# Kernel tuning notes

Measured on AMD Instinct MI355X. Metric: run time of the kernel, lower is better.

Reference implementation:

```python
import jax, jax.numpy as jnp
import numpy as np

B, N, K_NEIGHBORS = 8, 2048, 16

def setup_inputs() -> dict:
    key = jax.random.key(0)
    k1, k2, k3 = jax.random.split(key, 3)
    distance_matrix = jax.random.uniform(k1, (B, N, N), dtype=jnp.float32)
    time_window_compatibility = jax.random.randint(k2, (B, N, N), 0, 2).astype(jnp.int32)
    depot = jax.random.randint(k3, (B, N), 0, 2).astype(jnp.int32)
    # graph.max_dist: per-batch max pairwise distance, broadcastable over [B,N,N]
    max_dist = jnp.max(distance_matrix.reshape(B, -1), axis=1).reshape(B, 1, 1)
    return {
        "distance_matrix": distance_matrix,
        "max_dist": max_dist,
        "time_window_compatibility": time_window_compatibility,
        "depot": depot,
        "num_neighbors_encoder": K_NEIGHBORS,
    }


def reference(distance_matrix, max_dist, time_window_compatibility, depot, num_neighbors_encoder):
    """Faithful JAX port of Actor.compute_encoder_mask.

    distance_matrix:            [B, N, N] float
    max_dist:                   [B, 1, 1] float
    time_window_compatibility:  [B, N, N] int 0/1
    depot:                      [B, N]    int 0/1
    num_neighbors_encoder:      python int (K)
    returns mask:               [B, N, N] float 0/1
    """
    dtype = distance_matrix.dtype
    b, n, _ = distance_matrix.shape

    twnc = (1 - time_window_compatibility).astype(dtype)          # time-window NON-compatibility
    diag = jnp.eye(n, dtype=dtype)                                  # [N,N], broadcasts over batch
    m = ((twnc + diag) > 0).astype(dtype)                           # blocked pairs for KNN

    # Push blocked pairs far away, then take K smallest distances per row.
    dist = distance_matrix * (1.0 - m) + m * max_dist * 10.0
    k = min(n, int(num_neighbors_encoder))
    neighbors_index = jax.lax.top_k(-dist, k)[1]                    # [B, N, K] smallest-dist indices

    # neighbors_mask[b,i,j] = 1 iff j is among the K nearest neighbors of i.
    bi = jnp.arange(b)[:, None, None]
    ii = jnp.arange(n)[None, :, None]
    neighbors_mask = jnp.zeros((b, n, n), dtype).at[bi, ii, neighbors_index].add(1.0)

    m2 = (twnc == 0).astype(dtype)                                  # time-window compatible pairs
    neighbs_time_mask = neighbors_mask * m2

    depot_f = depot.astype(dtype)
    depot_mask = ((depot_f[:, None, :] + depot_f[:, :, None]) > 0).astype(dtype)

    mask = ((neighbs_time_mask + depot_mask + diag) > 0).astype(dtype)
    return mask
```

## Files before the change

### kernel.cpp

```cpp
#include <hip/hip_runtime.h>
#include <stdint.h>

#define NN 2048
#define TPB 256
#define EPT 8
#define KNB 16
#define CAP 128
#define CAPPAD (CAP + 8)

static constexpr unsigned long long EXCL = ~0ull;
static constexpr unsigned long long T0KEY = ((unsigned long long)0x3D400000u) << 11;

__global__ __launch_bounds__(TPB) void encoder_mask_kernel(
    const float* __restrict__ D,
    const int*   __restrict__ TWC,
    const int*   __restrict__ depot,
    float*       __restrict__ out)
{
    const int row = blockIdx.x;
    const int b   = row >> 11;
    const int i   = row & (NN - 1);
    const int t   = threadIdx.x;
    const int j0  = t * EPT;

    float*       orow   = out + (size_t)row * NN;
    const int*   deprow = depot + b * NN;

    const int4 p0 = reinterpret_cast<const int4*>(deprow + j0)[0];
    const int4 p1 = reinterpret_cast<const int4*>(deprow + j0)[1];
    const int  depot_i = deprow[i];

    if (depot_i != 0) {
        const float4 ones = make_float4(1.f, 1.f, 1.f, 1.f);
        float4* o4 = reinterpret_cast<float4*>(orow + j0);
        o4[0] = ones;
        o4[1] = ones;
        return;
    }

    const float* drow = D   + (size_t)row * NN;
    const int*   trow = TWC + (size_t)row * NN;

    const float4 d0 = reinterpret_cast<const float4*>(drow + j0)[0];
    const float4 d1 = reinterpret_cast<const float4*>(drow + j0)[1];
    const int4   c0 = reinterpret_cast<const int4*>(trow + j0)[0];
    const int4   c1 = reinterpret_cast<const int4*>(trow + j0)[1];

    __shared__ unsigned long long cand[CAPPAD];
    __shared__ unsigned long long selq[TPB];
    __shared__ unsigned long long wpart[2][TPB / 64];
    __shared__ int cnt;

    selq[t] = 0ull;
    if (t < CAPPAD) cand[t] = EXCL;
    if (t == 0) cnt = 0;
    __syncthreads();

    const float dv[EPT] = {d0.x, d0.y, d0.z, d0.w, d1.x, d1.y, d1.z, d1.w};
    const int   cv[EPT] = {c0.x, c0.y, c0.z, c0.w, c1.x, c1.y, c1.z, c1.w};

    unsigned long long key[EPT];
    #pragma unroll
    for (int k = 0; k < EPT; ++k) {
        const int j = j0 + k;
        const bool excl = (cv[k] == 0) | (j == i);
        key[k] = excl ? EXCL
                      : ((((unsigned long long)__float_as_uint(dv[k])) << 11) |
                         (unsigned long long)(unsigned)j);
    }

    int nloc = 0;
    #pragma unroll
    for (int k = 0; k < EPT; ++k) nloc += (key[k] < T0KEY) ? 1 : 0;

    if (nloc > 0) {
        int idx = atomicAdd(&cnt, nloc);
        #pragma unroll
        for (int k = 0; k < EPT; ++k) {
            if (key[k] < T0KEY) {
                if (idx < CAP) cand[idx] = key[k];
                ++idx;
            }
        }
    }
    __syncthreads();

    const int c = cnt;

    if (c >= KNB && c <= CAP) {
        if (t < c) {
            const unsigned long long mykey = cand[t];
            int rank = 0;
            const int cround = (c + 7) & ~7;
            #pragma unroll 1
            for (int q = 0; q < cround; q += 8) {
                const ulonglong2 a0 = *reinterpret_cast<const ulonglong2*>(&cand[q]);
                const ulonglong2 a1 = *reinterpret_cast<const ulonglong2*>(&cand[q + 2]);
                const ulonglong2 a2 = *reinterpret_cast<const ulonglong2*>(&cand[q + 4]);
                const ulonglong2 a3 = *reinterpret_cast<const ulonglong2*>(&cand[q + 6]);
                rank += (a0.x < mykey) ? 1 : 0;
                rank += (a0.y < mykey) ? 1 : 0;
                rank += (a1.x < mykey) ? 1 : 0;
                rank += (a1.y < mykey) ? 1 : 0;
                rank += (a2.x < mykey) ? 1 : 0;
                rank += (a2.y < mykey) ? 1 : 0;
                rank += (a3.x < mykey) ? 1 : 0;
                rank += (a3.y < mykey) ? 1 : 0;
            }
            if (rank < KNB) {
                reinterpret_cast<unsigned char*>(selq)[(int)(mykey & 2047u)] = 1;
            }
        }
    } else {
        const int wave = t >> 6;
        const int lane = t & 63;
        unsigned long long lmin = key[0];
        #pragma unroll
        for (int k = 1; k < EPT; ++k) lmin = (key[k] < lmin) ? key[k] : lmin;

        #pragma unroll 1
        for (int it = 0; it < KNB; ++it) {
            unsigned long long w = lmin;
            #pragma unroll
            for (int off = 32; off >= 1; off >>= 1) {
                const unsigned long long o = __shfl_xor(w, off);
                w = (o < w) ? o : w;
            }
            const int p = it & 1;
            if (lane == 0) wpart[p][wave] = w;
            __syncthreads();
            unsigned long long g = wpart[p][0];
            {
                const unsigned long long g1 = wpart[p][1];
                const unsigned long long g2 = wpart[p][2];
                const unsigned long long g3 = wpart[p][3];
                g = (g1 < g) ? g1 : g;
                g = (g2 < g) ? g2 : g;
                g = (g3 < g) ? g3 : g;
            }
            if (g == EXCL) break;
            const int jwin = (int)(g & 2047u);
            if (t == 0) reinterpret_cast<unsigned char*>(selq)[jwin] = 1;
            if (lmin == g) {
                unsigned long long nm = EXCL;
                #pragma unroll
                for (int k = 0; k < EPT; ++k) {
                    if (key[k] == g) key[k] = EXCL;
                    nm = (key[k] < nm) ? key[k] : nm;
                }
                lmin = nm;
            }
        }
    }
    __syncthreads();

    const unsigned long long selbits = selq[t];
    const int dpv[EPT] = {p0.x, p0.y, p0.z, p0.w, p1.x, p1.y, p1.z, p1.w};

    float ov[EPT];
    #pragma unroll
    for (int k = 0; k < EPT; ++k) {
        const int j = j0 + k;
        const bool sel = ((selbits >> (8 * k)) & 0xffull) != 0ull;
        const bool one = (dpv[k] != 0) | (j == i) | sel;
        ov[k] = one ? 1.0f : 0.0f;
    }
    float4* o4 = reinterpret_cast<float4*>(orow + j0);
    o4[0] = make_float4(ov[0], ov[1], ov[2], ov[3]);
    o4[1] = make_float4(ov[4], ov[5], ov[6], ov[7]);
}

extern "C" void kernel_launch(void* const* d_in, const int* in_sizes, int n_in,
                              void* d_out, int out_size, void* d_ws, size_t ws_size,
                              hipStream_t stream) {
    const float* D     = (const float*)d_in[0];
    const int*   TWC   = (const int*)d_in[2];
    const int*   depot = (const int*)d_in[3];

    float* outp = (float*)d_out;
    const int rows = in_sizes[3];

    encoder_mask_kernel<<<rows, TPB, 0, stream>>>(D, TWC, depot, outp);
}
```

Measured before the change: 48.14 us.

## Process four rows per block with register prefetch of the next row

Each block now handles four consecutive rows instead of one. While the current row's top-k selection runs, the distance and compatibility data for the next non-depot row are loaded into registers. Shared candidate and selection buffers are double-buffered by parity so one barrier per row suffices. This aims to hide global load latency and cut per-block launch overhead. The cost is a quarter as many blocks and serialized rows within a block, which reduces parallelism and latency hiding across blocks.

```diff
diff --git a/kernel.cpp b/kernel.cpp
--- a/kernel.cpp
+++ b/kernel.cpp
@@ -7,167 +7,201 @@
 #define KNB 16
 #define CAP 128
 #define CAPPAD (CAP + 8)
+#define RPB 4
 
 static constexpr unsigned long long EXCL = ~0ull;
 static constexpr unsigned long long T0KEY = ((unsigned long long)0x3D400000u) << 11;
 
-__global__ __launch_bounds__(TPB) void encoder_mask_kernel(
+__global__ __launch_bounds__(TPB, 8) void encoder_mask_kernel(
     const float* __restrict__ D,
     const int*   __restrict__ TWC,
     const int*   __restrict__ depot,
     float*       __restrict__ out)
 {
-    const int row = blockIdx.x;
-    const int b   = row >> 11;
-    const int i   = row & (NN - 1);
-    const int t   = threadIdx.x;
-    const int j0  = t * EPT;
-
-    float*       orow   = out + (size_t)row * NN;
-    const int*   deprow = depot + b * NN;
+    const int g      = blockIdx.x;
+    const int r_base = g * RPB;
+    const int b      = r_base >> 11;
+    const int i_base = r_base & (NN - 1);
+    const int t      = threadIdx.x;
+    const int j0     = t * EPT;
+
+    const int* deprow = depot + b * NN;
 
     const int4 p0 = reinterpret_cast<const int4*>(deprow + j0)[0];
     const int4 p1 = reinterpret_cast<const int4*>(deprow + j0)[1];
-    const int  depot_i = deprow[i];
-
-    if (depot_i != 0) {
-        const float4 ones = make_float4(1.f, 1.f, 1.f, 1.f);
-        float4* o4 = reinterpret_cast<float4*>(orow + j0);
-        o4[0] = ones;
-        o4[1] = ones;
-        return;
+
+    int depmask = 0;
+    #pragma unroll
+    for (int r = 0; r < RPB; ++r)
+        depmask |= (deprow[i_base + r] != 0) ? (1 << r) : 0;
+
+    __shared__ unsigned long long cand[2][CAPPAD];
+    __shared__ unsigned long long selq[2][TPB];
+    __shared__ unsigned long long wpart[2][TPB / 64];
+    __shared__ int cnt[2];
+
+    selq[0][t] = 0ull;
+    selq[1][t] = 0ull;
+    if (t < CAPPAD) { cand[0][t] = EXCL; cand[1][t] = EXCL; }
+    if (t == 0) { cnt[0] = 0; cnt[1] = 0; }
+
+    int next = 0;
+    while (next < RPB && ((depmask >> next) & 1)) ++next;
+
+    float4 d0, d1; int4 c0, c1;
+    if (next < RPB) {
+        const float* drow = D   + (size_t)(r_base + next) * NN;
+        const int*   trow = TWC + (size_t)(r_base + next) * NN;
+        d0 = reinterpret_cast<const float4*>(drow + j0)[0];
+        d1 = reinterpret_cast<const float4*>(drow + j0)[1];
+        c0 = reinterpret_cast<const int4*>(trow + j0)[0];
+        c1 = reinterpret_cast<const int4*>(trow + j0)[1];
     }
-
-    const float* drow = D   + (size_t)row * NN;
-    const int*   trow = TWC + (size_t)row * NN;
-
-    const float4 d0 = reinterpret_cast<const float4*>(drow + j0)[0];
-    const float4 d1 = reinterpret_cast<const float4*>(drow + j0)[1];
-    const int4   c0 = reinterpret_cast<const int4*>(trow + j0)[0];
-    const int4   c1 = reinterpret_cast<const int4*>(trow + j0)[1];
-
-    __shared__ unsigned long long cand[CAPPAD];
-    __shared__ unsigned long long selq[TPB];
-    __shared__ unsigned long long wpart[2][TPB / 64];
-    __shared__ int cnt;
-
-    selq[t] = 0ull;
-    if (t < CAPPAD) cand[t] = EXCL;
-    if (t == 0) cnt = 0;
     __syncthreads();
 
-    const float dv[EPT] = {d0.x, d0.y, d0.z, d0.w, d1.x, d1.y, d1.z, d1.w};
-    const int   cv[EPT] = {c0.x, c0.y, c0.z, c0.w, c1.x, c1.y, c1.z, c1.w};
-
-    unsigned long long key[EPT];
-    #pragma unroll
-    for (int k = 0; k < EPT; ++k) {
-        const int j = j0 + k;
-        const bool excl = (cv[k] == 0) | (j == i);
-        key[k] = excl ? EXCL
-                      : ((((unsigned long long)__float_as_uint(dv[k])) << 11) |
-                         (unsigned long long)(unsigned)j);
-    }
-
-    int nloc = 0;
-    #pragma unroll
-    for (int k = 0; k < EPT; ++k) nloc += (key[k] < T0KEY) ? 1 : 0;
-
-    if (nloc > 0) {
-        int idx = atomicAdd(&cnt, nloc);
+    int parity = 0;
+    #pragma unroll 1
+    for (int r = 0; r < RPB; ++r) {
+        const int row  = r_base + r;
+        float*    orow = out + (size_t)row * NN;
+
+        if ((depmask >> r) & 1) {
+            const float4 ones = make_float4(1.f, 1.f, 1.f, 1.f);
+            float4* o4 = reinterpret_cast<float4*>(orow + j0);
+            o4[0] = ones;
+            o4[1] = ones;
+            continue;
+        }
+
+        const float dv[EPT] = {d0.x, d0.y, d0.z, d0.w, d1.x, d1.y, d1.z, d1.w};
+        const int   cv[EPT] = {c0.x, c0.y, c0.z, c0.w, c1.x, c1.y, c1.z, c1.w};
+        const int   i = i_base + r;
+
+        unsigned long long key[EPT];
         #pragma unroll
         for (int k = 0; k < EPT; ++k) {
-            if (key[k] < T0KEY) {
-                if (idx < CAP) cand[idx] = key[k];
-                ++idx;
+            const int j = j0 + k;
+            const bool excl = (cv[k] == 0) | (j == i);
+            key[k] = excl ? EXCL
+                          : ((((unsigned long long)__float_as_uint(dv[k])) << 11) |
+                             (unsigned long long)(unsigned)j);
+        }
+
+        ++next;
+        while (next < RPB && ((depmask >> next) & 1)) ++next;
+        if (next < RPB) {
+            const float* drow = D   + (size_t)(r_base + next) * NN;
+            const int*   trow = TWC + (size_t)(r_base + next) * NN;
+            d0 = reinterpret_cast<const float4*>(drow + j0)[0];
+            d1 = reinterpret_cast<const float4*>(drow + j0)[1];
+            c0 = reinterpret_cast<const int4*>(trow + j0)[0];
+            c1 = reinterpret_cast<const int4*>(trow + j0)[1];
+        }
+
+        int nloc = 0;
+        #pragma unroll
+        for (int k = 0; k < EPT; ++k) nloc += (key[k] < T0KEY) ? 1 : 0;
+        if (nloc > 0) {
+            int idx = atomicAdd(&cnt[parity], nloc);
+            #pragma unroll
+            for (int k = 0; k < EPT; ++k) {
+                if (key[k] < T0KEY) {
+                    if (idx < CAP) cand[parity][idx] = key[k];
+                    ++idx;
+                }
             }
         }
+        __syncthreads();
+
+        const int c = cnt[parity];
+        if (c >= KNB && c <= CAP) {
+            if (t < c) {
+                const unsigned long long mykey = cand[parity][t];
+                int rank = 0;
+                const int cround = (c + 7) & ~7;
+                #pragma unroll 1
+                for (int q = 0; q < cround; q += 8) {
+                    const ulonglong2 a0 = *reinterpret_cast<const ulonglong2*>(&cand[parity][q]);
+                    const ulonglong2 a1 = *reinterpret_cast<const ulonglong2*>(&cand[parity][q + 2]);
+                    const ulonglong2 a2 = *reinterpret_cast<const ulonglong2*>(&cand[parity][q + 4]);
+                    const ulonglong2 a3 = *reinterpret_cast<const ulonglong2*>(&cand[parity][q + 6]);
+                    rank += (a0.x < mykey) ? 1 : 0;
+                    rank += (a0.y < mykey) ? 1 : 0;
+                    rank += (a1.x < mykey) ? 1 : 0;
+                    rank += (a1.y < mykey) ? 1 : 0;
+                    rank += (a2.x < mykey) ? 1 : 0;
+                    rank += (a2.y < mykey) ? 1 : 0;
+                    rank += (a3.x < mykey) ? 1 : 0;
+                    rank += (a3.y < mykey) ? 1 : 0;
+                }
+                if (rank < KNB) {
+                    reinterpret_cast<unsigned char*>(selq[parity])[(int)(mykey & 2047u)] = 1;
+                }
+            }
+        } else {
+            const int wave = t >> 6;
+            const int lane = t & 63;
+            unsigned long long lmin = key[0];
+            #pragma unroll
+            for (int k = 1; k < EPT; ++k) lmin = (key[k] < lmin) ? key[k] : lmin;
+
+            #pragma unroll 1
+            for (int it = 0; it < KNB; ++it) {
+                unsigned long long w = lmin;
+                #pragma unroll
+                for (int off = 32; off >= 1; off >>= 1) {
+                    const unsigned long long o = __shfl_xor(w, off);
+                    w = (o < w) ? o : w;
+                }
+                const int pp = it & 1;
+                if (lane == 0) wpart[pp][wave] = w;
+                __syncthreads();
+                unsigned long long gm = wpart[pp][0];
+                {
+                    const unsigned long long g1 = wpart[pp][1];
+                    const unsigned long long g2 = wpart[pp][2];
+                    const unsigned long long g3 = wpart[pp][3];
+                    gm = (g1 < gm) ? g1 : gm;
+                    gm = (g2 < gm) ? g2 : gm;
+                    gm = (g3 < gm) ? g3 : gm;
+                }
+                if (gm == EXCL) break;
+                if (t == 0)
+                    reinterpret_cast<unsigned char*>(selq[parity])[(int)(gm & 2047u)] = 1;
+                if (lmin == gm) {
+                    unsigned long long nm = EXCL;
+                    #pragma unroll
+                    for (int k = 0; k < EPT; ++k) {
+                        if (key[k] == gm) key[k] = EXCL;
+                        nm = (key[k] < nm) ? key[k] : nm;
+                    }
+                    lmin = nm;
+                }
+            }
+        }
+        __syncthreads();
+
+        const unsigned long long selbits = selq[parity][t];
+
+        selq[parity][t] = 0ull;
+        if (t < CAPPAD) cand[parity][t] = EXCL;
+        if (t == 0) cnt[parity] = 0;
+
+        const int dpv[EPT] = {p0.x, p0.y, p0.z, p0.w, p1.x, p1.y, p1.z, p1.w};
+        float ov[EPT];
+        #pragma unroll
+        for (int k = 0; k < EPT; ++k) {
+            const int j = j0 + k;
+            const bool sel = ((selbits >> (8 * k)) & 0xffull) != 0ull;
+            const bool one = (dpv[k] != 0) | (j == i) | sel;
+            ov[k] = one ? 1.0f : 0.0f;
+        }
+        float4* o4 = reinterpret_cast<float4*>(orow + j0);
+        o4[0] = make_float4(ov[0], ov[1], ov[2], ov[3]);
+        o4[1] = make_float4(ov[4], ov[5], ov[6], ov[7]);
+
+        parity ^= 1;
     }
-    __syncthreads();
-
-    const int c = cnt;
-
-    if (c >= KNB && c <= CAP) {
-        if (t < c) {
-            const unsigned long long mykey = cand[t];
-            int rank = 0;
-            const int cround = (c + 7) & ~7;
-            #pragma unroll 1
-            for (int q = 0; q < cround; q += 8) {
-                const ulonglong2 a0 = *reinterpret_cast<const ulonglong2*>(&cand[q]);
-                const ulonglong2 a1 = *reinterpret_cast<const ulonglong2*>(&cand[q + 2]);
-                const ulonglong2 a2 = *reinterpret_cast<const ulonglong2*>(&cand[q + 4]);
-                const ulonglong2 a3 = *reinterpret_cast<const ulonglong2*>(&cand[q + 6]);
-                rank += (a0.x < mykey) ? 1 : 0;
-                rank += (a0.y < mykey) ? 1 : 0;
-                rank += (a1.x < mykey) ? 1 : 0;
-                rank += (a1.y < mykey) ? 1 : 0;
-                rank += (a2.x < mykey) ? 1 : 0;
-                rank += (a2.y < mykey) ? 1 : 0;
-                rank += (a3.x < mykey) ? 1 : 0;
-                rank += (a3.y < mykey) ? 1 : 0;
-            }
-            if (rank < KNB) {
-                reinterpret_cast<unsigned char*>(selq)[(int)(mykey & 2047u)] = 1;
-            }
-        }
-    } else {
-        const int wave = t >> 6;
-        const int lane = t & 63;
-        unsigned long long lmin = key[0];
-        #pragma unroll
-        for (int k = 1; k < EPT; ++k) lmin = (key[k] < lmin) ? key[k] : lmin;
-
-        #pragma unroll 1
-        for (int it = 0; it < KNB; ++it) {
-            unsigned long long w = lmin;
-            #pragma unroll
-            for (int off = 32; off >= 1; off >>= 1) {
-                const unsigned long long o = __shfl_xor(w, off);
-                w = (o < w) ? o : w;
-            }
-            const int p = it & 1;
-            if (lane == 0) wpart[p][wave] = w;
-            __syncthreads();
-            unsigned long long g = wpart[p][0];
-            {
-                const unsigned long long g1 = wpart[p][1];
-                const unsigned long long g2 = wpart[p][2];
-                const unsigned long long g3 = wpart[p][3];
-                g = (g1 < g) ? g1 : g;
-                g = (g2 < g) ? g2 : g;
-                g = (g3 < g) ? g3 : g;
-            }
-            if (g == EXCL) break;
-            const int jwin = (int)(g & 2047u);
-            if (t == 0) reinterpret_cast<unsigned char*>(selq)[jwin] = 1;
-            if (lmin == g) {
-                unsigned long long nm = EXCL;
-                #pragma unroll
-                for (int k = 0; k < EPT; ++k) {
-                    if (key[k] == g) key[k] = EXCL;
-                    nm = (key[k] < nm) ? key[k] : nm;
-                }
-                lmin = nm;
-            }
-        }
-    }
-    __syncthreads();
-
-    const unsigned long long selbits = selq[t];
-    const int dpv[EPT] = {p0.x, p0.y, p0.z, p0.w, p1.x, p1.y, p1.z, p1.w};
-
-    float ov[EPT];
-    #pragma unroll
-    for (int k = 0; k < EPT; ++k) {
-        const int j = j0 + k;
-        const bool sel = ((selbits >> (8 * k)) & 0xffull) != 0ull;
-        const bool one = (dpv[k] != 0) | (j == i) | sel;
-        ov[k] = one ? 1.0f : 0.0f;
-    }
-    float4* o4 = reinterpret_cast<float4*>(orow + j0);
-    o4[0] = make_float4(ov[0], ov[1], ov[2], ov[3]);
-    o4[1] = make_float4(ov[4], ov[5], ov[6], ov[7]);
 }
 
 extern "C" void kernel_launch(void* const* d_in, const int* in_sizes, int n_in,
@@ -180,5 +214,5 @@
     float* outp = (float*)d_out;
     const int rows = in_sizes[3];
 
-    encoder_mask_kernel<<<rows, TPB, 0, stream>>>(D, TWC, depot, outp);
+    encoder_mask_kernel<<<rows / RPB, TPB, 0, stream>>>(D, TWC, depot, outp);
 }
```

Measured after the change: 89.52 us. +86.0%, slower.
